# Kernel optimization log

Measured on AMD Instinct MI355X. Metric: run time of the kernel, lower is better.

The kernel has to match this reference:

```python
import jax, jax.numpy as jnp
import numpy as np

N_NODES = 50000
N_EDGES = 800000
D = 64  # in_dim = hidden_dim = out_dim


def gcn_conv(x, edge_index, W, b, num_nodes):
    """PyG GCNConv: x' = D^{-1/2} (A + I) D^{-1/2} (x W) + b."""
    h = x @ W  # [N, out]
    # add self-loops
    loop = jnp.arange(num_nodes, dtype=edge_index.dtype)
    row = jnp.concatenate([edge_index[0], loop])  # sources j
    col = jnp.concatenate([edge_index[1], loop])  # targets i
    # symmetric normalization
    ones = jnp.ones(row.shape[0], dtype=h.dtype)
    deg = jax.ops.segment_sum(ones, col, num_segments=num_nodes)
    dinv = jnp.where(deg > 0, jax.lax.rsqrt(deg), 0.0)
    norm = dinv[row] * dinv[col]  # [E+N]
    # gather -> scale -> scatter-add
    msg = h[row] * norm[:, None]
    out = jax.ops.segment_sum(msg, col, num_segments=num_nodes)
    return out + b


def setup_inputs() -> dict:
    key = jax.random.key(0)
    k = jax.random.split(key, 6)
    x = jax.random.normal(k[0], (N_NODES, D), dtype=jnp.float32)
    edge_index = jax.random.randint(k[1], (2, N_EDGES), 0, N_NODES, dtype=jnp.int64)
    s = 1.0 / np.sqrt(D)
    W1 = jax.random.uniform(k[2], (D, D), jnp.float32, -s, s)
    b1 = jnp.zeros((D,), jnp.float32)
    W2 = jax.random.uniform(k[3], (D, D), jnp.float32, -s, s)
    b2 = jnp.zeros((D,), jnp.float32)
    return {"x": x, "edge_index": edge_index, "W1": W1, "b1": b1, "W2": W2, "b2": b2}


def reference(x, edge_index, W1, b1, W2, b2):
    h = gcn_conv(x, edge_index, W1, b1, N_NODES)
    h = jax.nn.relu(h)
    out = gcn_conv(h, edge_index, W2, b2, N_NODES)
    return out
```

## Files before the change

### kernel.cpp

```cpp
#include <hip/hip_runtime.h>
#include <hip/hip_fp16.h>

#define N_NODES 50000
#define N_EDGES 800000
#define RANGES 8
#define SLICES 16
#define NPB (N_NODES / RANGES)
#define I4S (N_EDGES / SLICES / 4)
#define CAP 48
#define GEMM_BLOCKS (N_NODES / 16)
#define DINV_BLOCKS ((N_NODES + 255) / 256)

__global__ __launch_bounds__(1024)
void count_kernel(const int* __restrict__ col, unsigned char* __restrict__ cnt8) {
    __shared__ int cur[NPB];
    int tid = threadIdx.x;
    int r = blockIdx.x & (RANGES - 1), s = blockIdx.x >> 3;
    int lo = r * NPB;
    for (int i = tid; i < NPB; i += 1024) cur[i] = 0;
    __syncthreads();
    const int4* c4 = (const int4*)col;
    for (int i = s * I4S + tid; i < (s + 1) * I4S; i += 1024) {
        int4 c = c4[i];
        int dx = c.x - lo, dy = c.y - lo, dz = c.z - lo, dw = c.w - lo;
        if ((unsigned)dx < NPB) atomicAdd(&cur[dx], 1);
        if ((unsigned)dy < NPB) atomicAdd(&cur[dy], 1);
        if ((unsigned)dz < NPB) atomicAdd(&cur[dz], 1);
        if ((unsigned)dw < NPB) atomicAdd(&cur[dw], 1);
    }
    __syncthreads();
    for (int i = tid; i < NPB; i += 1024)
        cnt8[(size_t)(lo + i) * SLICES + s] = (unsigned char)min(cur[i], 255);
}

__device__ __forceinline__ void gemm_body(int blk, const float* __restrict__ X,
                                          const float* __restrict__ W,
                                          __half* __restrict__ H) {
    int tid = threadIdx.x, lane = tid & 63, wv = tid >> 6;
    float w[64];
    #pragma unroll
    for (int k = 0; k < 64; ++k) w[k] = W[k * 64 + lane];
    int node0 = blk * 16 + wv * 4;
    #pragma unroll
    for (int r = 0; r < 4; ++r) {
        int node = node0 + r;
        float xv = X[(size_t)node * 64 + lane];
        float a0 = 0.f, a1 = 0.f;
        #pragma unroll
        for (int k = 0; k < 64; k += 2) {
            a0 = fmaf(__shfl(xv, k, 64),     w[k],     a0);
            a1 = fmaf(__shfl(xv, k + 1, 64), w[k + 1], a1);
        }
        H[(size_t)node * 64 + lane] = __float2half(a0 + a1);
    }
}

__device__ __forceinline__ int bytesum4(unsigned v) {
    return (v & 0xFF) + ((v >> 8) & 0xFF) + ((v >> 16) & 0xFF) + (v >> 24);
}

__global__ __launch_bounds__(256)
void gemm_dinv_kernel(const unsigned char* __restrict__ cnt8,
                      int* __restrict__ cntf, float* __restrict__ dinv,
                      unsigned short* __restrict__ dinv16u,
                      const float* __restrict__ X, const float* __restrict__ W,
                      __half* __restrict__ H) {
    if (blockIdx.x < GEMM_BLOCKS) {
        gemm_body(blockIdx.x, X, W, H);
    } else {
        int node = (blockIdx.x - GEMM_BLOCKS) * 256 + threadIdx.x;
        if (node < N_NODES) {
            uint4 c = ((const uint4*)cnt8)[node];
            int n = bytesum4(c.x) + bytesum4(c.y) + bytesum4(c.z) + bytesum4(c.w);
            float di = rsqrtf((float)(n + 1));
            cntf[node] = min(n, CAP);
            dinv[node] = di;
            dinv16u[node] = __half_as_ushort(__float2half(di));
        }
    }
}

__global__ __launch_bounds__(1024)
void place_kernel(const int* __restrict__ row, const int* __restrict__ col,
                  const unsigned char* __restrict__ cnt8,
                  const unsigned short* __restrict__ dinv16u,
                  unsigned int* __restrict__ epk) {
    __shared__ int cur[NPB];
    int tid = threadIdx.x;
    int r = blockIdx.x & (RANGES - 1), s = blockIdx.x >> 3;
    int lo = r * NPB;
    for (int i = tid; i < NPB; i += 1024) {
        uint4 c = ((const uint4*)cnt8)[lo + i];
        unsigned w0 = c.x, w1 = c.y, w2 = c.z, w3 = c.w;
        int base = 0;
        if (s >= 4)  { base += bytesum4(w0); }
        else         { for (int k = 0; k < s; ++k)      base += (w0 >> (8*k)) & 0xFF; }
        if (s >= 8)  { base += bytesum4(w1); }
        else if (s > 4)  { for (int k = 0; k < s-4; ++k)  base += (w1 >> (8*k)) & 0xFF; }
        if (s >= 12) { base += bytesum4(w2); }
        else if (s > 8)  { for (int k = 0; k < s-8; ++k)  base += (w2 >> (8*k)) & 0xFF; }
        if (s > 12)  { for (int k = 0; k < s-12; ++k) base += (w3 >> (8*k)) & 0xFF; }
        cur[i] = base;
    }
    __syncthreads();
    const int4* c4 = (const int4*)col;
    const int4* r4 = (const int4*)row;
    for (int i = s * I4S + tid; i < (s + 1) * I4S; i += 1024) {
        int4 c  = c4[i];
        int4 rr = r4[i];
        int dx = c.x - lo, dy = c.y - lo, dz = c.z - lo, dw = c.w - lo;
        if ((unsigned)dx < NPB) {
            int p = atomicAdd(&cur[dx], 1);
            if (p < CAP) epk[(size_t)(lo + dx) * CAP + p]
                = (unsigned)rr.x | ((unsigned)dinv16u[rr.x] << 16);
        }
        if ((unsigned)dy < NPB) {
            int p = atomicAdd(&cur[dy], 1);
            if (p < CAP) epk[(size_t)(lo + dy) * CAP + p]
                = (unsigned)rr.y | ((unsigned)dinv16u[rr.y] << 16);
        }
        if ((unsigned)dz < NPB) {
            int p = atomicAdd(&cur[dz], 1);
            if (p < CAP) epk[(size_t)(lo + dz) * CAP + p]
                = (unsigned)rr.z | ((unsigned)dinv16u[rr.z] << 16);
        }
        if ((unsigned)dw < NPB) {
            int p = atomicAdd(&cur[dw], 1);
            if (p < CAP) epk[(size_t)(lo + dw) * CAP + p]
                = (unsigned)rr.w | ((unsigned)dinv16u[rr.w] << 16);
        }
    }
}

template<int FUSE>
__global__ __launch_bounds__(256)
void gather_kernel(const __half* __restrict__ H, const int* __restrict__ cntf,
                   const unsigned int* __restrict__ epk,
                   const float* __restrict__ dinv,
                   const float* __restrict__ bias, const float* __restrict__ W2,
                   void* __restrict__ outp) {
    __shared__ float xg[4][64];
    int tid = threadIdx.x, lane = tid & 63, wv = tid >> 6;
    int node = blockIdx.x * 4 + wv;
    int n = cntf[node];
    float di = dinv[node];
    unsigned int e = 0;
    if (lane < n) e = epk[(size_t)node * CAP + lane];
    if (lane == n)
        e = (unsigned)node
          | ((unsigned)__half_as_ushort(__float2half(di)) << 16);
    int m = n + 1;
    int grp = lane >> 3, off = lane & 7;
    const float4* H4 = (const float4*)H;
    float a0=0.f,a1=0.f,a2=0.f,a3=0.f,a4=0.f,a5=0.f,a6=0.f,a7=0.f;
    int nr = (m + 15) & ~15;
    for (int j = 0; j < nr; j += 16) {
        unsigned qa = (unsigned)__shfl((int)e, j + grp, 64);
        unsigned qb = (unsigned)__shfl((int)e, j + 8 + grp, 64);
        float4 va = H4[(size_t)(qa & 0xFFFFu) * 8 + off];
        float4 vb = H4[(size_t)(qb & 0xFFFFu) * 8 + off];
        float wa = __half2float(__ushort_as_half((unsigned short)(qa >> 16)));
        float wb = __half2float(__ushort_as_half((unsigned short)(qb >> 16)));
        const __half2* ha = (const __half2*)&va;
        float2 f0 = __half22float2(ha[0]), f1 = __half22float2(ha[1]);
        float2 f2 = __half22float2(ha[2]), f3 = __half22float2(ha[3]);
        a0 = fmaf(wa, f0.x, a0); a1 = fmaf(wa, f0.y, a1);
        a2 = fmaf(wa, f1.x, a2); a3 = fmaf(wa, f1.y, a3);
        a4 = fmaf(wa, f2.x, a4); a5 = fmaf(wa, f2.y, a5);
        a6 = fmaf(wa, f3.x, a6); a7 = fmaf(wa, f3.y, a7);
        const __half2* hb = (const __half2*)&vb;
        f0 = __half22float2(hb[0]); f1 = __half22float2(hb[1]);
        f2 = __half22float2(hb[2]); f3 = __half22float2(hb[3]);
        a0 = fmaf(wb, f0.x, a0); a1 = fmaf(wb, f0.y, a1);
        a2 = fmaf(wb, f1.x, a2); a3 = fmaf(wb, f1.y, a3);
        a4 = fmaf(wb, f2.x, a4); a5 = fmaf(wb, f2.y, a5);
        a6 = fmaf(wb, f3.x, a6); a7 = fmaf(wb, f3.y, a7);
    }
    a0 += __shfl_xor(a0, 8, 64); a0 += __shfl_xor(a0, 16, 64); a0 += __shfl_xor(a0, 32, 64);
    a1 += __shfl_xor(a1, 8, 64); a1 += __shfl_xor(a1, 16, 64); a1 += __shfl_xor(a1, 32, 64);
    a2 += __shfl_xor(a2, 8, 64); a2 += __shfl_xor(a2, 16, 64); a2 += __shfl_xor(a2, 32, 64);
    a3 += __shfl_xor(a3, 8, 64); a3 += __shfl_xor(a3, 16, 64); a3 += __shfl_xor(a3, 32, 64);
    a4 += __shfl_xor(a4, 8, 64); a4 += __shfl_xor(a4, 16, 64); a4 += __shfl_xor(a4, 32, 64);
    a5 += __shfl_xor(a5, 8, 64); a5 += __shfl_xor(a5, 16, 64); a5 += __shfl_xor(a5, 32, 64);
    a6 += __shfl_xor(a6, 8, 64); a6 += __shfl_xor(a6, 16, 64); a6 += __shfl_xor(a6, 32, 64);
    a7 += __shfl_xor(a7, 8, 64); a7 += __shfl_xor(a7, 16, 64); a7 += __shfl_xor(a7, 32, 64);
    if (lane < 8) {
        xg[wv][lane * 8 + 0] = a0; xg[wv][lane * 8 + 1] = a1;
        xg[wv][lane * 8 + 2] = a2; xg[wv][lane * 8 + 3] = a3;
        xg[wv][lane * 8 + 4] = a4; xg[wv][lane * 8 + 5] = a5;
        xg[wv][lane * 8 + 6] = a6; xg[wv][lane * 8 + 7] = a7;
    }
    float sum = xg[wv][lane];
    float gval = di * sum + bias[lane];
    if constexpr (FUSE) {
        gval = fmaxf(gval, 0.f);
        float wc[64];
        #pragma unroll
        for (int k = 0; k < 64; ++k) wc[k] = W2[k * 64 + lane];
        float o0 = 0.f, o1 = 0.f;
        #pragma unroll
        for (int k = 0; k < 64; k += 2) {
            o0 = fmaf(__shfl(gval, k, 64),     wc[k],     o0);
            o1 = fmaf(__shfl(gval, k + 1, 64), wc[k + 1], o1);
        }
        ((__half*)outp)[(size_t)node * 64 + lane] = __float2half(o0 + o1);
    } else {
        ((float*)outp)[(size_t)node * 64 + lane] = gval;
    }
}

extern "C" void kernel_launch(void* const* d_in, const int* in_sizes, int n_in,
                              void* d_out, int out_size, void* d_ws, size_t ws_size,
                              hipStream_t stream) {
    const float* x   = (const float*)d_in[0];
    const int*   ei  = (const int*)d_in[1];
    const int*   row = ei;
    const int*   col = ei + N_EDGES;
    const float* W1  = (const float*)d_in[2];
    const float* b1  = (const float*)d_in[3];
    const float* W2  = (const float*)d_in[4];
    const float* b2  = (const float*)d_in[5];
    float* out = (float*)d_out;

    char* p = (char*)d_ws;
    __half* h  = (__half*)p;            p += (size_t)N_NODES * 64 * 2;
    __half* h2 = (__half*)p;            p += (size_t)N_NODES * 64 * 2;
    unsigned char*  cnt8    = (unsigned char*)p;  p += (size_t)N_NODES * SLICES;
    unsigned int*   epk     = (unsigned int*)p;   p += (size_t)N_NODES * CAP * 4;
    float*          dinv    = (float*)p;          p += (size_t)N_NODES * 4;
    unsigned short* dinv16u = (unsigned short*)p; p += (size_t)N_NODES * 2;
    int*            cntf    = (int*)p;            p += (size_t)N_NODES * 4;

    count_kernel<<<RANGES * SLICES, 1024, 0, stream>>>(col, cnt8);
    gemm_dinv_kernel<<<GEMM_BLOCKS + DINV_BLOCKS, 256, 0, stream>>>(
        cnt8, cntf, dinv, dinv16u, x, W1, h);
    place_kernel<<<RANGES * SLICES, 1024, 0, stream>>>(row, col, cnt8, dinv16u, epk);
    gather_kernel<1><<<N_NODES / 4, 256, 0, stream>>>(h, cntf, epk, dinv, b1, W2, h2);
    gather_kernel<0><<<N_NODES / 4, 256, 0, stream>>>(h2, cntf, epk, dinv, b2, nullptr, out);
}
```

Before: 219.7 us.

## Widen count slices to 64 and restructure gather into half2 batched loads

Raises the edge slice count from 16 to 64, so the per-node byte counter array grows to 64 bytes per node and count/place kernels launch four times as many blocks with smaller edge chunks each. The gather kernel is rewritten so each half-wave loads one half2 per lane per neighbour, with batches of 8 or 16 independent loads issued before any accumulation. This replaces the float4-per-8-lane scheme and its 24-shuffle reduction through shared memory with a single xor shuffle plus a lane remap. It aims for more memory-level parallelism in the gather and better occupancy in the edge-binning kernels, at the cost of more, smaller loads and a larger counter array.

```diff
diff --git a/kernel.cpp b/kernel.cpp
--- a/kernel.cpp
+++ b/kernel.cpp
@@ -4,12 +4,16 @@
 #define N_NODES 50000
 #define N_EDGES 800000
 #define RANGES 8
-#define SLICES 16
+#define SLICES 64
 #define NPB (N_NODES / RANGES)
 #define I4S (N_EDGES / SLICES / 4)
 #define CAP 48
 #define GEMM_BLOCKS (N_NODES / 16)
 #define DINV_BLOCKS ((N_NODES + 255) / 256)
+
+__device__ __forceinline__ int bytesum4(unsigned v) {
+    return (v & 0xFF) + ((v >> 8) & 0xFF) + ((v >> 16) & 0xFF) + (v >> 24);
+}
 
 __global__ __launch_bounds__(1024)
 void count_kernel(const int* __restrict__ col, unsigned char* __restrict__ cnt8) {
@@ -55,10 +59,6 @@
     }
 }
 
-__device__ __forceinline__ int bytesum4(unsigned v) {
-    return (v & 0xFF) + ((v >> 8) & 0xFF) + ((v >> 16) & 0xFF) + (v >> 24);
-}
-
 __global__ __launch_bounds__(256)
 void gemm_dinv_kernel(const unsigned char* __restrict__ cnt8,
                       int* __restrict__ cntf, float* __restrict__ dinv,
@@ -70,8 +70,12 @@
     } else {
         int node = (blockIdx.x - GEMM_BLOCKS) * 256 + threadIdx.x;
         if (node < N_NODES) {
-            uint4 c = ((const uint4*)cnt8)[node];
-            int n = bytesum4(c.x) + bytesum4(c.y) + bytesum4(c.z) + bytesum4(c.w);
+            const uint4* c16 = (const uint4*)(cnt8 + (size_t)node * SLICES);
+            uint4 c0 = c16[0], c1 = c16[1], c2 = c16[2], c3 = c16[3];
+            int n = bytesum4(c0.x) + bytesum4(c0.y) + bytesum4(c0.z) + bytesum4(c0.w)
+                  + bytesum4(c1.x) + bytesum4(c1.y) + bytesum4(c1.z) + bytesum4(c1.w)
+                  + bytesum4(c2.x) + bytesum4(c2.y) + bytesum4(c2.z) + bytesum4(c2.w)
+                  + bytesum4(c3.x) + bytesum4(c3.y) + bytesum4(c3.z) + bytesum4(c3.w);
             float di = rsqrtf((float)(n + 1));
             cntf[node] = min(n, CAP);
             dinv[node] = di;
@@ -89,17 +93,15 @@
     int tid = threadIdx.x;
     int r = blockIdx.x & (RANGES - 1), s = blockIdx.x >> 3;
     int lo = r * NPB;
+    int fullw = s >> 2, part = s & 3;
     for (int i = tid; i < NPB; i += 1024) {
-        uint4 c = ((const uint4*)cnt8)[lo + i];
-        unsigned w0 = c.x, w1 = c.y, w2 = c.z, w3 = c.w;
+        const unsigned* cw = (const unsigned*)(cnt8 + (size_t)(lo + i) * SLICES);
         int base = 0;
-        if (s >= 4)  { base += bytesum4(w0); }
-        else         { for (int k = 0; k < s; ++k)      base += (w0 >> (8*k)) & 0xFF; }
-        if (s >= 8)  { base += bytesum4(w1); }
-        else if (s > 4)  { for (int k = 0; k < s-4; ++k)  base += (w1 >> (8*k)) & 0xFF; }
-        if (s >= 12) { base += bytesum4(w2); }
-        else if (s > 8)  { for (int k = 0; k < s-8; ++k)  base += (w2 >> (8*k)) & 0xFF; }
-        if (s > 12)  { for (int k = 0; k < s-12; ++k) base += (w3 >> (8*k)) & 0xFF; }
+        for (int w = 0; w < fullw; ++w) base += bytesum4(cw[w]);
+        if (part) {
+            unsigned pw = cw[fullw];
+            for (int k = 0; k < part; ++k) base += (pw >> (8 * k)) & 0xFF;
+        }
         cur[i] = base;
     }
     __syncthreads();
@@ -132,6 +134,26 @@
     }
 }
 
+template<int K>
+__device__ __forceinline__ void agg_batch(int e, int slot0, const __half2* H2,
+                                          int sub, int half, float& ax, float& ay) {
+    unsigned q[K];
+    __half2  v[K];
+    #pragma unroll
+    for (int k = 0; k < K; ++k)
+        q[k] = (unsigned)__shfl(e, slot0 + 2 * k + half, 64);
+    #pragma unroll
+    for (int k = 0; k < K; ++k)
+        v[k] = H2[(size_t)(q[k] & 0xFFFFu) * 32 + sub];
+    #pragma unroll
+    for (int k = 0; k < K; ++k) {
+        float w = __half2float(__ushort_as_half((unsigned short)(q[k] >> 16)));
+        float2 f = __half22float2(v[k]);
+        ax = fmaf(w, f.x, ax);
+        ay = fmaf(w, f.y, ay);
+    }
+}
+
 template<int FUSE>
 __global__ __launch_bounds__(256)
 void gather_kernel(const __half* __restrict__ H, const int* __restrict__ cntf,
@@ -139,58 +161,34 @@
                    const float* __restrict__ dinv,
                    const float* __restrict__ bias, const float* __restrict__ W2,
                    void* __restrict__ outp) {
-    __shared__ float xg[4][64];
     int tid = threadIdx.x, lane = tid & 63, wv = tid >> 6;
+    int half = lane >> 5, sub = lane & 31;
     int node = blockIdx.x * 4 + wv;
     int n = cntf[node];
     float di = dinv[node];
-    unsigned int e = 0;
-    if (lane < n) e = epk[(size_t)node * CAP + lane];
+    int e = 0;
+    if (lane < n) e = (int)epk[(size_t)node * CAP + lane];
     if (lane == n)
-        e = (unsigned)node
-          | ((unsigned)__half_as_ushort(__float2half(di)) << 16);
+        e = (int)((unsigned)node
+          | ((unsigned)__half_as_ushort(__float2half(di)) << 16));
     int m = n + 1;
-    int grp = lane >> 3, off = lane & 7;
-    const float4* H4 = (const float4*)H;
-    float a0=0.f,a1=0.f,a2=0.f,a3=0.f,a4=0.f,a5=0.f,a6=0.f,a7=0.f;
-    int nr = (m + 15) & ~15;
-    for (int j = 0; j < nr; j += 16) {
-        unsigned qa = (unsigned)__shfl((int)e, j + grp, 64);
-        unsigned qb = (unsigned)__shfl((int)e, j + 8 + grp, 64);
-        float4 va = H4[(size_t)(qa & 0xFFFFu) * 8 + off];
-        float4 vb = H4[(size_t)(qb & 0xFFFFu) * 8 + off];
-        float wa = __half2float(__ushort_as_half((unsigned short)(qa >> 16)));
-        float wb = __half2float(__ushort_as_half((unsigned short)(qb >> 16)));
-        const __half2* ha = (const __half2*)&va;
-        float2 f0 = __half22float2(ha[0]), f1 = __half22float2(ha[1]);
-        float2 f2 = __half22float2(ha[2]), f3 = __half22float2(ha[3]);
-        a0 = fmaf(wa, f0.x, a0); a1 = fmaf(wa, f0.y, a1);
-        a2 = fmaf(wa, f1.x, a2); a3 = fmaf(wa, f1.y, a3);
-        a4 = fmaf(wa, f2.x, a4); a5 = fmaf(wa, f2.y, a5);
-        a6 = fmaf(wa, f3.x, a6); a7 = fmaf(wa, f3.y, a7);
-        const __half2* hb = (const __half2*)&vb;
-        f0 = __half22float2(hb[0]); f1 = __half22float2(hb[1]);
-        f2 = __half22float2(hb[2]); f3 = __half22float2(hb[3]);
-        a0 = fmaf(wb, f0.x, a0); a1 = fmaf(wb, f0.y, a1);
-        a2 = fmaf(wb, f1.x, a2); a3 = fmaf(wb, f1.y, a3);
-        a4 = fmaf(wb, f2.x, a4); a5 = fmaf(wb, f2.y, a5);
-        a6 = fmaf(wb, f3.x, a6); a7 = fmaf(wb, f3.y, a7);
-    }
-    a0 += __shfl_xor(a0, 8, 64); a0 += __shfl_xor(a0, 16, 64); a0 += __shfl_xor(a0, 32, 64);
-    a1 += __shfl_xor(a1, 8, 64); a1 += __shfl_xor(a1, 16, 64); a1 += __shfl_xor(a1, 32, 64);
-    a2 += __shfl_xor(a2, 8, 64); a2 += __shfl_xor(a2, 16, 64); a2 += __shfl_xor(a2, 32, 64);
-    a3 += __shfl_xor(a3, 8, 64); a3 += __shfl_xor(a3, 16, 64); a3 += __shfl_xor(a3, 32, 64);
-    a4 += __shfl_xor(a4, 8, 64); a4 += __shfl_xor(a4, 16, 64); a4 += __shfl_xor(a4, 32, 64);
-    a5 += __shfl_xor(a5, 8, 64); a5 += __shfl_xor(a5, 16, 64); a5 += __shfl_xor(a5, 32, 64);
-    a6 += __shfl_xor(a6, 8, 64); a6 += __shfl_xor(a6, 16, 64); a6 += __shfl_xor(a6, 32, 64);
-    a7 += __shfl_xor(a7, 8, 64); a7 += __shfl_xor(a7, 16, 64); a7 += __shfl_xor(a7, 32, 64);
-    if (lane < 8) {
-        xg[wv][lane * 8 + 0] = a0; xg[wv][lane * 8 + 1] = a1;
-        xg[wv][lane * 8 + 2] = a2; xg[wv][lane * 8 + 3] = a3;
-        xg[wv][lane * 8 + 4] = a4; xg[wv][lane * 8 + 5] = a5;
-        xg[wv][lane * 8 + 6] = a6; xg[wv][lane * 8 + 7] = a7;
-    }
-    float sum = xg[wv][lane];
+    const __half2* H2 = (const __half2*)H;
+    float ax = 0.f, ay = 0.f;
+    if (m <= 16) {
+        agg_batch<8>(e, 0, H2, sub, half, ax, ay);
+    } else {
+        agg_batch<16>(e, 0, H2, sub, half, ax, ay);
+        if (m > 32) {
+            int nr = (m + 15) & ~15;
+            for (int b = 32; b < nr; b += 16)
+                agg_batch<8>(e, b, H2, sub, half, ax, ay);
+        }
+    }
+    ax += __shfl_xor(ax, 32, 64);
+    ay += __shfl_xor(ay, 32, 64);
+    float cx = __shfl(ax, lane >> 1, 64);
+    float cy = __shfl(ay, lane >> 1, 64);
+    float sum = (lane & 1) ? cy : cx;
     float gval = di * sum + bias[lane];
     if constexpr (FUSE) {
         gval = fmaxf(gval, 0.f);
```

New measurement: 237.9 us. 8.3% more time.
